# Performance work log

Hardware: AMD Instinct MI355X
Metric: run time of the kernel (lower is better)

The kernel has to match this reference:

```python
import jax, jax.numpy as jnp
import numpy as np

H, D, DS, CZ, S, B = 16, 24, 384, 128, 512, 1
EPS = 1e-5


def setup_inputs() -> dict:
    key = jax.random.key(0)
    ks = jax.random.split(key, 12)
    sc = lambda fan: 1.0 / np.sqrt(fan)
    inp = {
        's': jax.random.normal(ks[0], (B, S, DS), jnp.float32),
        'z': jax.random.normal(ks[1], (B, S, S, CZ), jnp.float32),
        'seq_mask': jnp.zeros((B, 1, 1, S), jnp.float32),
        'q_w': jax.random.normal(ks[2], (H * D, DS), jnp.float32) * sc(DS),
        'q_b': jax.random.normal(ks[3], (H * D,), jnp.float32) * 0.02,
        'k_w': jax.random.normal(ks[4], (H * D, DS), jnp.float32) * sc(DS),
        'v_w': jax.random.normal(ks[5], (H * D, DS), jnp.float32) * sc(DS),
        'g_w': jax.random.normal(ks[6], (H * D, DS), jnp.float32) * sc(DS),
        'o_w': jax.random.normal(ks[7], (DS, H * D), jnp.float32) * sc(H * D),
        'z_ln_w': jnp.ones((CZ,), jnp.float32),
        'z_ln_b': jnp.zeros((CZ,), jnp.float32),
        'z_w': jax.random.normal(ks[8], (H, CZ), jnp.float32) * sc(CZ),
    }
    return inp


def _layer_norm(x, w, b):
    mu = jnp.mean(x, axis=-1, keepdims=True)
    var = jnp.mean(jnp.square(x - mu), axis=-1, keepdims=True)
    return (x - mu) * jax.lax.rsqrt(var + EPS) * w + b


def reference(s, z, seq_mask, q_w, q_b, k_w, v_w, g_w, o_w, z_ln_w, z_ln_b, z_w):
    b, n, _ = s.shape
    # fused QKV projection (q has bias, k/v do not)
    q = (s @ q_w.T + q_b).reshape(b, n, H, D).transpose(0, 2, 1, 3)  # [B,H,S,D]
    k = (s @ k_w.T).reshape(b, n, H, D).transpose(0, 2, 1, 3)
    v = (s @ v_w.T).reshape(b, n, H, D).transpose(0, 2, 1, 3)
    # pair bias: layernorm(z) -> linear to H -> permute to [B,H,S,S]
    bias = _layer_norm(z, z_ln_w, z_ln_b) @ z_w.T          # [B,S,S,H]
    bias = bias.transpose(0, 3, 1, 2)                      # [B,H,S,S]
    bias = bias + seq_mask
    scores = jnp.einsum('bhqd,bhkd->bhqk', q, k) * (D ** -0.5) + bias
    attn = jax.nn.softmax(scores, axis=-1)
    o = jnp.einsum('bhqk,bhkd->bhqd', attn, v)             # [B,H,S,D]
    o = o.transpose(0, 2, 1, 3).reshape(b, n, H * D)
    g = jax.nn.sigmoid(s @ g_w.T)                          # gating
    return (o * g) @ o_w.T                                 # [B,S,DS]
```

## Files before the change

### kernel.cpp

```cpp
#include <hip/hip_runtime.h>

#define H 16
#define D 24
#define DS 384
#define CZ 128
#define S 512
#define EPSV 1e-5f
#define TR 64

__global__ __launch_bounds__(256) void proj_kernel(
    const float* __restrict__ s, const float* __restrict__ q_w, const float* __restrict__ q_b,
    const float* __restrict__ k_w, const float* __restrict__ v_w, const float* __restrict__ g_w,
    float* __restrict__ Q, float* __restrict__ K, float* __restrict__ VT, float* __restrict__ G)
{
    const int b = blockIdx.x;
    const int mat = b / 48;
    const int t = b % 48;
    const int by = t / 6, bx = t % 6;
    const float* w = (mat == 0) ? q_w : (mat == 1) ? k_w : (mat == 2) ? v_w : g_w;

    __shared__ float As[32][68];
    __shared__ float Ws[32][68];

    const int tid = threadIdx.x;
    const int tx = tid & 15, ty = tid >> 4;
    const int r8 = tid >> 3;
    const int c4 = tid & 7;

    float acc[4][4] = {};
    for (int kc = 0; kc < DS; kc += 32) {
        __syncthreads();
#pragma unroll
        for (int pass = 0; pass < 2; ++pass) {
            int r = r8 + pass * 32;
            float4 sv = *(const float4*)(s + (by * 64 + r) * DS + kc + c4 * 4);
            float4 wv = *(const float4*)(w + (bx * 64 + r) * DS + kc + c4 * 4);
            As[c4 * 4 + 0][r] = sv.x; As[c4 * 4 + 1][r] = sv.y;
            As[c4 * 4 + 2][r] = sv.z; As[c4 * 4 + 3][r] = sv.w;
            Ws[c4 * 4 + 0][r] = wv.x; Ws[c4 * 4 + 1][r] = wv.y;
            Ws[c4 * 4 + 2][r] = wv.z; Ws[c4 * 4 + 3][r] = wv.w;
        }
        __syncthreads();
#pragma unroll
        for (int k = 0; k < 32; ++k) {
            float4 a4 = *(const float4*)&As[k][ty * 4];
            float4 b4 = *(const float4*)&Ws[k][tx * 4];
            acc[0][0] += a4.x * b4.x; acc[0][1] += a4.x * b4.y; acc[0][2] += a4.x * b4.z; acc[0][3] += a4.x * b4.w;
            acc[1][0] += a4.y * b4.x; acc[1][1] += a4.y * b4.y; acc[1][2] += a4.y * b4.z; acc[1][3] += a4.y * b4.w;
            acc[2][0] += a4.z * b4.x; acc[2][1] += a4.z * b4.y; acc[2][2] += a4.z * b4.z; acc[2][3] += a4.z * b4.w;
            acc[3][0] += a4.w * b4.x; acc[3][1] += a4.w * b4.y; acc[3][2] += a4.w * b4.z; acc[3][3] += a4.w * b4.w;
        }
    }

    const int r0 = by * 64 + ty * 4;
    const int c0 = bx * 64 + tx * 4;
    if (mat == 2) {
#pragma unroll
        for (int ii = 0; ii < 4; ++ii)
#pragma unroll
            for (int jj = 0; jj < 4; ++jj)
                VT[(c0 + jj) * S + (r0 + ii)] = acc[ii][jj];
    } else {
        float* dst = (mat == 0) ? Q : (mat == 1) ? K : G;
#pragma unroll
        for (int ii = 0; ii < 4; ++ii) {
            float4 v;
            v.x = acc[ii][0]; v.y = acc[ii][1]; v.z = acc[ii][2]; v.w = acc[ii][3];
            if (mat == 0) {
                v.x += q_b[c0 + 0]; v.y += q_b[c0 + 1]; v.z += q_b[c0 + 2]; v.w += q_b[c0 + 3];
            } else if (mat == 3) {
                v.x = 1.f / (1.f + __expf(-v.x)); v.y = 1.f / (1.f + __expf(-v.y));
                v.z = 1.f / (1.f + __expf(-v.z)); v.w = 1.f / (1.f + __expf(-v.w));
            }
            *(float4*)(dst + (r0 + ii) * DS + c0) = v;
        }
    }
}

__global__ __launch_bounds__(256) void score_kernel(
    const float* __restrict__ z, const float* __restrict__ seq_mask,
    const float* __restrict__ z_ln_w, const float* __restrict__ z_ln_b,
    const float* __restrict__ z_w,
    const float* __restrict__ Q, const float* __restrict__ K,
    float* __restrict__ scores)
{
    const int b = blockIdx.x;
    const int q = b >> 3;
    const int j0 = (b & 7) * TR;
    const int tid = threadIdx.x;

    __shared__ float zs[TR][CZ + 4];
    __shared__ float a_s[H][CZ + 4];
    __shared__ float qrow[DS];
    __shared__ float mu_s[TR], rs_s[TR];
    __shared__ float Ah[H], Bh[H];

    for (int i = tid; i < H * CZ; i += 256) {
        int h = i >> 7, c = i & 127;
        a_s[h][c] = z_ln_w[c] * z_w[h * CZ + c];
    }
    {
        const float4* zg = (const float4*)(z + ((long)q * S + j0) * CZ);
        for (int i = tid; i < TR * (CZ / 4); i += 256) {
            int row = i >> 5, c4 = i & 31;
            float4 v = zg[row * 32 + c4];
            *(float4*)&zs[row][c4 * 4] = v;
        }
    }
    for (int i = tid; i < DS; i += 256) qrow[i] = Q[q * DS + i];
    __syncthreads();

    if (tid < H) {
        float A = 0.f, B = 0.f;
        for (int c = 0; c < CZ; ++c) {
            A += a_s[tid][c];
            B += z_ln_b[c] * z_w[tid * CZ + c];
        }
        Ah[tid] = A; Bh[tid] = B;
    }
    {
        int row = tid >> 2, qr = tid & 3;
        const float4* zr = (const float4*)&zs[row][qr * 32];
        float sum = 0.f, sq = 0.f;
#pragma unroll
        for (int t = 0; t < 8; ++t) {
            float4 f = zr[t];
            sum += f.x + f.y + f.z + f.w;
            sq += f.x * f.x + f.y * f.y + f.z * f.z + f.w * f.w;
        }
        sum += __shfl_xor(sum, 1); sum += __shfl_xor(sum, 2);
        sq  += __shfl_xor(sq, 1);  sq  += __shfl_xor(sq, 2);
        if (qr == 0) {
            float mu = sum * (1.f / 128.f);
            float var = sq * (1.f / 128.f) - mu * mu;
            mu_s[row] = mu;
            rs_s[row] = 1.f / sqrtf(var + EPSV);
        }
    }
    __syncthreads();

    const int rg = tid >> 3;
    const int hg = tid & 7;
    const int r0 = rg * 2, h0 = hg * 2;

    float dza[2][2] = {};
#pragma unroll 8
    for (int c4 = 0; c4 < 32; ++c4) {
        float4 z0 = *(const float4*)&zs[r0][c4 * 4];
        float4 z1 = *(const float4*)&zs[r0 + 1][c4 * 4];
        float4 a0 = *(const float4*)&a_s[h0][c4 * 4];
        float4 a1 = *(const float4*)&a_s[h0 + 1][c4 * 4];
        dza[0][0] += z0.x * a0.x + z0.y * a0.y + z0.z * a0.z + z0.w * a0.w;
        dza[0][1] += z0.x * a1.x + z0.y * a1.y + z0.z * a1.z + z0.w * a1.w;
        dza[1][0] += z1.x * a0.x + z1.y * a0.y + z1.z * a0.z + z1.w * a0.w;
        dza[1][1] += z1.x * a1.x + z1.y * a1.y + z1.z * a1.z + z1.w * a1.w;
    }

    float pk[2][2];
#pragma unroll
    for (int i = 0; i < 2; ++i) {
        const float* kr = K + (long)(j0 + r0 + i) * DS;
#pragma unroll
        for (int jj = 0; jj < 2; ++jj) {
            const float4* k4 = (const float4*)(kr + (h0 + jj) * D);
            const float4* q4 = (const float4*)(qrow + (h0 + jj) * D);
            float acc = 0.f;
#pragma unroll
            for (int t = 0; t < 6; ++t) {
                float4 kv = k4[t];
                float4 qv = q4[t];
                acc += kv.x * qv.x + kv.y * qv.y + kv.z * qv.z + kv.w * qv.w;
            }
            pk[i][jj] = acc;
        }
    }

    const float scale = 0.2041241452319315f;
#pragma unroll
    for (int i = 0; i < 2; ++i) {
        int j = j0 + r0 + i;
        float mu = mu_s[r0 + i], rs = rs_s[r0 + i];
        float mk = seq_mask[j];
#pragma unroll
        for (int jj = 0; jj < 2; ++jj) {
            int h = h0 + jj;
            float bias = rs * dza[i][jj] - mu * rs * Ah[h] + Bh[h];
            scores[((q << 4) + h) * S + j] = pk[i][jj] * scale + bias + mk;
        }
    }
}

__global__ __launch_bounds__(256) void spv_kernel(
    const float* __restrict__ scores, const float* __restrict__ VT,
    const float* __restrict__ G, float* __restrict__ og)
{
    const int q = blockIdx.x;
    const int tid = threadIdx.x;
    const int wv = tid >> 6;
    const int lane = tid & 63;

    __shared__ float sc[H][S + 4];
    __shared__ float opart[4][DS];
    __shared__ float inv_l[H];

    for (int i = tid; i < H * (S / 4); i += 256) {
        int row = i >> 7, f4 = i & 127;
        float4 v = ((const float4*)(scores + ((q << 4) + row) * S))[f4];
        *(float4*)&sc[row][f4 * 4] = v;
    }
    __syncthreads();

#pragma unroll
    for (int i = 0; i < 4; ++i) {
        int h = wv * 4 + i;
        float m = -1e30f;
        for (int j = lane; j < S; j += 64) m = fmaxf(m, sc[h][j]);
#pragma unroll
        for (int mk = 1; mk < 64; mk <<= 1) m = fmaxf(m, __shfl_xor(m, mk));
        float sum = 0.f;
        for (int j = lane; j < S; j += 64) {
            float p = __expf(sc[h][j] - m);
            sc[h][j] = p;
            sum += p;
        }
#pragma unroll
        for (int mk = 1; mk < 64; mk <<= 1) sum += __shfl_xor(sum, mk);
        if (lane == 0) inv_l[h] = 1.f / sum;
    }
    __syncthreads();

#pragma unroll
    for (int ii = 0; ii < 6; ++ii) {
        int idx = ii * 64 + lane;
        int h = idx / 24;
        float acc = 0.f;
        const float4* vt4 = (const float4*)(VT + idx * S + wv * 128);
        const float4* sc4 = (const float4*)&sc[h][wv * 128];
#pragma unroll
        for (int t = 0; t < 32; ++t) {
            float4 p = sc4[t];
            float4 v = vt4[t];
            acc += p.x * v.x + p.y * v.y + p.z * v.z + p.w * v.w;
        }
        opart[wv][idx] = acc;
    }
    __syncthreads();
    for (int i = tid; i < DS; i += 256) {
        float o = opart[0][i] + opart[1][i] + opart[2][i] + opart[3][i];
        int h = i / 24;
        og[q * DS + i] = o * inv_l[h] * G[q * DS + i];
    }
}

__global__ __launch_bounds__(256) void out_kernel(
    const float* __restrict__ og, const float* __restrict__ o_w, float* __restrict__ out)
{
    const int b = blockIdx.x;
    const int by = b / 6, bx = b % 6;

    __shared__ float As[32][68];
    __shared__ float Ws[32][68];

    const int tid = threadIdx.x;
    const int tx = tid & 15, ty = tid >> 4;
    const int r8 = tid >> 3;
    const int c4 = tid & 7;

    float acc[4][4] = {};
    for (int kc = 0; kc < DS; kc += 32) {
        __syncthreads();
#pragma unroll
        for (int pass = 0; pass < 2; ++pass) {
            int r = r8 + pass * 32;
            float4 sv = *(const float4*)(og + (by * 64 + r) * DS + kc + c4 * 4);
            float4 wvv = *(const float4*)(o_w + (bx * 64 + r) * DS + kc + c4 * 4);
            As[c4 * 4 + 0][r] = sv.x; As[c4 * 4 + 1][r] = sv.y;
            As[c4 * 4 + 2][r] = sv.z; As[c4 * 4 + 3][r] = sv.w;
            Ws[c4 * 4 + 0][r] = wvv.x; Ws[c4 * 4 + 1][r] = wvv.y;
            Ws[c4 * 4 + 2][r] = wvv.z; Ws[c4 * 4 + 3][r] = wvv.w;
        }
        __syncthreads();
#pragma unroll
        for (int k = 0; k < 32; ++k) {
            float4 a4 = *(const float4*)&As[k][ty * 4];
            float4 b4 = *(const float4*)&Ws[k][tx * 4];
            acc[0][0] += a4.x * b4.x; acc[0][1] += a4.x * b4.y; acc[0][2] += a4.x * b4.z; acc[0][3] += a4.x * b4.w;
            acc[1][0] += a4.y * b4.x; acc[1][1] += a4.y * b4.y; acc[1][2] += a4.y * b4.z; acc[1][3] += a4.y * b4.w;
            acc[2][0] += a4.z * b4.x; acc[2][1] += a4.z * b4.y; acc[2][2] += a4.z * b4.z; acc[2][3] += a4.z * b4.w;
            acc[3][0] += a4.w * b4.x; acc[3][1] += a4.w * b4.y; acc[3][2] += a4.w * b4.z; acc[3][3] += a4.w * b4.w;
        }
    }

    const int r0 = by * 64 + ty * 4;
    const int c0 = bx * 64 + tx * 4;
#pragma unroll
    for (int ii = 0; ii < 4; ++ii) {
        float4 v;
        v.x = acc[ii][0]; v.y = acc[ii][1]; v.z = acc[ii][2]; v.w = acc[ii][3];
        *(float4*)(out + (r0 + ii) * DS + c0) = v;
    }
}

extern "C" void kernel_launch(void* const* d_in, const int* in_sizes, int n_in,
                              void* d_out, int out_size, void* d_ws, size_t ws_size,
                              hipStream_t stream)
{
    const float* s      = (const float*)d_in[0];
    const float* z      = (const float*)d_in[1];
    const float* mask   = (const float*)d_in[2];
    const float* q_w    = (const float*)d_in[3];
    const float* q_b    = (const float*)d_in[4];
    const float* k_w    = (const float*)d_in[5];
    const float* v_w    = (const float*)d_in[6];
    const float* g_w    = (const float*)d_in[7];
    const float* o_w    = (const float*)d_in[8];
    const float* z_ln_w = (const float*)d_in[9];
    const float* z_ln_b = (const float*)d_in[10];
    const float* z_w    = (const float*)d_in[11];

    float* Q  = (float*)d_ws;
    float* K  = Q + S * DS;
    float* VT = K + S * DS;
    float* G  = VT + S * DS;
    float* og = G + S * DS;
    float* scores = og + S * DS;

    hipLaunchKernelGGL(proj_kernel, dim3(192), dim3(256), 0, stream,
                       s, q_w, q_b, k_w, v_w, g_w, Q, K, VT, G);
    hipLaunchKernelGGL(score_kernel, dim3(4096), dim3(256), 0, stream,
                       z, mask, z_ln_w, z_ln_b, z_w, Q, K, scores);
    hipLaunchKernelGGL(spv_kernel, dim3(S), dim3(256), 0, stream,
                       scores, VT, G, og);
    hipLaunchKernelGGL(out_kernel, dim3(48), dim3(256), 0, stream,
                       og, o_w, (float*)d_out);
}
```

Before: 377.5 us.

## Restructure pair-bias score kernel to register-resident z with split-channel reduction

The score kernel no longer stages the 64x128 z tile in shared memory. Each wave now loads a 32-channel slice of z per row into registers, computes partial LN statistics and partial z·(ln_w*z_w) dot products for all 16 heads, then reduces the partials across waves through shared memory. The A/B head constants are computed in parallel with shuffles rather than by 16 serial threads, and scores are staged through shared memory so they can be written to global with coalesced float4 stores. This aims to cut shared-memory traffic and serial work, but it raises register pressure and adds partial-sum buffers.

Result: faster. 349.3 us (-7.5%).

```diff
diff --git a/kernel.cpp b/kernel.cpp
--- a/kernel.cpp
+++ b/kernel.cpp
@@ -6,7 +6,6 @@
 #define CZ 128
 #define S 512
 #define EPSV 1e-5f
-#define TR 64
 
 __global__ __launch_bounds__(256) void proj_kernel(
     const float* __restrict__ s, const float* __restrict__ q_w, const float* __restrict__ q_b,
@@ -86,107 +85,106 @@
 {
     const int b = blockIdx.x;
     const int q = b >> 3;
-    const int j0 = (b & 7) * TR;
+    const int j0 = (b & 7) * 64;
     const int tid = threadIdx.x;
-
-    __shared__ float zs[TR][CZ + 4];
+    const int w = tid >> 6;
+    const int lane = tid & 63;
+
     __shared__ float a_s[H][CZ + 4];
+    __shared__ float AhBh[2][H];
     __shared__ float qrow[DS];
-    __shared__ float mu_s[TR], rs_s[TR];
-    __shared__ float Ah[H], Bh[H];
-
-    for (int i = tid; i < H * CZ; i += 256) {
-        int h = i >> 7, c = i & 127;
-        a_s[h][c] = z_ln_w[c] * z_w[h * CZ + c];
-    }
+    __shared__ float stats[4][2][68];
+    __shared__ float opart[4][H][68];
+    __shared__ float buf[H][68];
+
     {
-        const float4* zg = (const float4*)(z + ((long)q * S + j0) * CZ);
-        for (int i = tid; i < TR * (CZ / 4); i += 256) {
-            int row = i >> 5, c4 = i & 31;
-            float4 v = zg[row * 32 + c4];
-            *(float4*)&zs[row][c4 * 4] = v;
-        }
+        const int h = tid >> 4;
+        const int c8 = (tid & 15) * 8;
+        float A = 0.f, Bv = 0.f;
+#pragma unroll
+        for (int p = 0; p < 2; ++p) {
+            float4 wz = *(const float4*)(z_w + h * CZ + c8 + p * 4);
+            float4 lw = *(const float4*)(z_ln_w + c8 + p * 4);
+            float4 lb = *(const float4*)(z_ln_b + c8 + p * 4);
+            float4 a;
+            a.x = lw.x * wz.x; a.y = lw.y * wz.y; a.z = lw.z * wz.z; a.w = lw.w * wz.w;
+            *(float4*)&a_s[h][c8 + p * 4] = a;
+            A += a.x + a.y + a.z + a.w;
+            Bv += lb.x * wz.x + lb.y * wz.y + lb.z * wz.z + lb.w * wz.w;
+        }
+#pragma unroll
+        for (int m = 1; m < 16; m <<= 1) {
+            A += __shfl_xor(A, m);
+            Bv += __shfl_xor(Bv, m);
+        }
+        if ((tid & 15) == 0) { AhBh[0][h] = A; AhBh[1][h] = Bv; }
     }
     for (int i = tid; i < DS; i += 256) qrow[i] = Q[q * DS + i];
     __syncthreads();
 
-    if (tid < H) {
-        float A = 0.f, B = 0.f;
-        for (int c = 0; c < CZ; ++c) {
-            A += a_s[tid][c];
-            B += z_ln_b[c] * z_w[tid * CZ + c];
-        }
-        Ah[tid] = A; Bh[tid] = B;
-    }
     {
-        int row = tid >> 2, qr = tid & 3;
-        const float4* zr = (const float4*)&zs[row][qr * 32];
-        float sum = 0.f, sq = 0.f;
+        const int c0 = w * 32;
+        const float* zr = z + ((long)q * S + j0 + lane) * CZ + c0;
+        float4 zf[8];
+#pragma unroll
+        for (int t = 0; t < 8; ++t) zf[t] = *(const float4*)(zr + t * 4);
+
+        float s1 = 0.f, s2 = 0.f;
 #pragma unroll
         for (int t = 0; t < 8; ++t) {
-            float4 f = zr[t];
-            sum += f.x + f.y + f.z + f.w;
-            sq += f.x * f.x + f.y * f.y + f.z * f.z + f.w * f.w;
-        }
-        sum += __shfl_xor(sum, 1); sum += __shfl_xor(sum, 2);
-        sq  += __shfl_xor(sq, 1);  sq  += __shfl_xor(sq, 2);
-        if (qr == 0) {
-            float mu = sum * (1.f / 128.f);
-            float var = sq * (1.f / 128.f) - mu * mu;
-            mu_s[row] = mu;
-            rs_s[row] = 1.f / sqrtf(var + EPSV);
-        }
-    }
-    __syncthreads();
-
-    const int rg = tid >> 3;
-    const int hg = tid & 7;
-    const int r0 = rg * 2, h0 = hg * 2;
-
-    float dza[2][2] = {};
-#pragma unroll 8
-    for (int c4 = 0; c4 < 32; ++c4) {
-        float4 z0 = *(const float4*)&zs[r0][c4 * 4];
-        float4 z1 = *(const float4*)&zs[r0 + 1][c4 * 4];
-        float4 a0 = *(const float4*)&a_s[h0][c4 * 4];
-        float4 a1 = *(const float4*)&a_s[h0 + 1][c4 * 4];
-        dza[0][0] += z0.x * a0.x + z0.y * a0.y + z0.z * a0.z + z0.w * a0.w;
-        dza[0][1] += z0.x * a1.x + z0.y * a1.y + z0.z * a1.z + z0.w * a1.w;
-        dza[1][0] += z1.x * a0.x + z1.y * a0.y + z1.z * a0.z + z1.w * a0.w;
-        dza[1][1] += z1.x * a1.x + z1.y * a1.y + z1.z * a1.z + z1.w * a1.w;
-    }
-
-    float pk[2][2];
-#pragma unroll
-    for (int i = 0; i < 2; ++i) {
-        const float* kr = K + (long)(j0 + r0 + i) * DS;
-#pragma unroll
-        for (int jj = 0; jj < 2; ++jj) {
-            const float4* k4 = (const float4*)(kr + (h0 + jj) * D);
-            const float4* q4 = (const float4*)(qrow + (h0 + jj) * D);
+            s1 += zf[t].x + zf[t].y + zf[t].z + zf[t].w;
+            s2 += zf[t].x * zf[t].x + zf[t].y * zf[t].y + zf[t].z * zf[t].z + zf[t].w * zf[t].w;
+        }
+        stats[w][0][lane] = s1;
+        stats[w][1][lane] = s2;
+
+#pragma unroll
+        for (int h = 0; h < H; ++h) {
             float acc = 0.f;
+#pragma unroll
+            for (int t = 0; t < 8; ++t) {
+                float4 a4 = *(const float4*)&a_s[h][c0 + t * 4];
+                acc += zf[t].x * a4.x + zf[t].y * a4.y + zf[t].z * a4.z + zf[t].w * a4.w;
+            }
+            opart[w][h][lane] = acc;
+        }
+    }
+    __syncthreads();
+
+    {
+        const int r = tid >> 2;
+        const int hq = tid & 3;
+        float s1 = stats[0][0][r] + stats[1][0][r] + stats[2][0][r] + stats[3][0][r];
+        float s2 = stats[0][1][r] + stats[1][1][r] + stats[2][1][r] + stats[3][1][r];
+        const float mu = s1 * (1.f / 128.f);
+        const float rs = rsqrtf(s2 * (1.f / 128.f) - mu * mu + EPSV);
+        const float mk = seq_mask[j0 + r];
+        const float scale = 0.2041241452319315f;
+        const float* krow = K + (long)(j0 + r) * DS;
+
+#pragma unroll
+        for (int i = 0; i < 4; ++i) {
+            const int h = hq * 4 + i;
+            float dza = opart[0][h][r] + opart[1][h][r] + opart[2][h][r] + opart[3][h][r];
+            const float4* k4 = (const float4*)(krow + h * D);
+            const float4* q4 = (const float4*)(qrow + h * D);
+            float qk = 0.f;
 #pragma unroll
             for (int t = 0; t < 6; ++t) {
                 float4 kv = k4[t];
                 float4 qv = q4[t];
-                acc += kv.x * qv.x + kv.y * qv.y + kv.z * qv.z + kv.w * qv.w;
+                qk += kv.x * qv.x + kv.y * qv.y + kv.z * qv.z + kv.w * qv.w;
             }
-            pk[i][jj] = acc;
-        }
-    }
-
-    const float scale = 0.2041241452319315f;
-#pragma unroll
-    for (int i = 0; i < 2; ++i) {
-        int j = j0 + r0 + i;
-        float mu = mu_s[r0 + i], rs = rs_s[r0 + i];
-        float mk = seq_mask[j];
-#pragma unroll
-        for (int jj = 0; jj < 2; ++jj) {
-            int h = h0 + jj;
-            float bias = rs * dza[i][jj] - mu * rs * Ah[h] + Bh[h];
-            scores[((q << 4) + h) * S + j] = pk[i][jj] * scale + bias + mk;
-        }
+            const float bias = rs * dza - mu * rs * AhBh[0][h] + AhBh[1][h];
+            buf[h][r] = qk * scale + bias + mk;
+        }
+    }
+    __syncthreads();
+
+    {
+        const int h = tid >> 4, j4 = tid & 15;
+        float4 v = *(const float4*)&buf[h][j4 * 4];
+        *(float4*)(scores + ((q << 4) + h) * S + j0 + j4 * 4) = v;
     }
 }
 
```
